# Optimization experiments

Hardware: AMD Instinct MI355X
Metric: run time of the kernel (lower is better)

## Reference

```python
import jax, jax.numpy as jnp
import numpy as np

WH, WW = 7, 7
N = WH * WW
C = 192
H = 6
D = C // H


def _rel_position_index(Wh, Ww):
    # double_step_seq(2*Ww-1, Wh, 1, Ww)
    seq1 = np.arange(0, (2 * Ww - 1) * Wh, 2 * Ww - 1)
    seq2 = np.arange(0, Ww, 1)
    coords = (seq1[:, None] + seq2[None, :]).reshape(1, -1)  # [1, Wh*Ww]
    idx = coords + coords.T                                   # [N, N]
    idx = idx[:, ::-1].copy()                                 # flip(1)
    return idx

REL_IDX = _rel_position_index(WH, WW)  # static int index [N, N]


def setup_inputs() -> dict:
    key = jax.random.key(0)
    ks = jax.random.split(key, 8)
    B = 8192
    nW = 64
    q = jax.random.normal(ks[0], (B, N, C), dtype=jnp.float32)
    kv = jax.random.normal(ks[1], (B, N, C), dtype=jnp.float32)
    mask = jnp.zeros((nW, N, N), dtype=jnp.float32)
    s = 0.02
    Wq = jax.random.normal(ks[2], (C, C), dtype=jnp.float32) * s
    bq = jnp.zeros((C,), dtype=jnp.float32)
    Wkv = jax.random.normal(ks[3], (2 * C, C), dtype=jnp.float32) * s
    bkv = jnp.zeros((2 * C,), dtype=jnp.float32)
    Wo = jax.random.normal(ks[4], (C, C), dtype=jnp.float32) * s
    bo = jnp.zeros((C,), dtype=jnp.float32)
    rpb_table = jax.random.normal(ks[5], ((2 * WH - 1) * (2 * WW - 1), H), dtype=jnp.float32) * s
    return {"q": q, "kv": kv, "mask": mask, "Wq": Wq, "bq": bq,
            "Wkv": Wkv, "bkv": bkv, "Wo": Wo, "bo": bo, "rpb_table": rpb_table}


def reference(q, kv, mask, Wq, bq, Wkv, bkv, Wo, bo, rpb_table):
    B, Nq, _ = q.shape
    Nk = kv.shape[1]
    scale = D ** -0.5
    qh = (q @ Wq.T + bq).reshape(B, Nq, H, D).transpose(0, 2, 1, 3)  # [B,H,Nq,D]
    kvh = (kv @ Wkv.T + bkv).reshape(B, Nk, 2, H, D)
    kh = kvh[:, :, 0].transpose(0, 2, 1, 3)  # [B,H,Nk,D]
    vh = kvh[:, :, 1].transpose(0, 2, 1, 3)
    attn = jnp.einsum('bhqd,bhkd->bhqk', qh * scale, kh)
    bias = rpb_table[REL_IDX.reshape(-1)].reshape(N, N, H).transpose(2, 0, 1)  # [H,N,N]
    attn = attn + bias[None]
    nW = mask.shape[0]
    attn = attn.reshape(B // nW, nW, H, Nq, Nk) + mask[None, :, None]
    attn = attn.reshape(B, H, Nq, Nk)
    attn = jax.nn.softmax(attn, axis=-1)
    x = jnp.einsum('bhqk,bhkd->bhqd', attn, vh).transpose(0, 2, 1, 3).reshape(B, Nq, C)
    return x @ Wo.T + bo
```

## Files before the change

### kernel.cpp

```cpp
#include <hip/hip_runtime.h>

#define NTOK 49
#define CDIM 192
#define NHEAD 6
#define HDIM 32

typedef float f32x4 __attribute__((ext_vector_type(4), may_alias));
typedef short b16x8 __attribute__((ext_vector_type(8), may_alias));
typedef short b16x4 __attribute__((ext_vector_type(4), may_alias));

__device__ __forceinline__ f32x4 MFMA(b16x8 a, b16x8 b, f32x4 c) {
  return __builtin_amdgcn_mfma_f32_16x16x32_bf16(a, b, c, 0, 0, 0);
}

__device__ __forceinline__ short f2bf(float f) {
  unsigned u = __builtin_bit_cast(unsigned, f);
  u += 0x7FFFu + ((u >> 16) & 1u);
  return (short)(u >> 16);
}

__device__ __forceinline__ int swz(int row, int col) {
  return row * CDIM + (col ^ ((row & 7) << 3));
}

__global__ void prep_w(const float* __restrict__ Wq, const float* __restrict__ Wkv,
                       const float* __restrict__ Wo, short* __restrict__ wsW) {
  const float scale = 0.17677669529663687f;
  int i = blockIdx.x * 256 + threadIdx.x;
  if (i >= 147456) return;
  float v;
  if (i < 36864)        v = Wq[i] * scale;
  else if (i < 110592)  v = Wkv[i - 36864];
  else                  v = Wo[i - 110592];
  wsW[i] = f2bf(v);
}

__global__ void prep_bias(const float* __restrict__ rpb, float* __restrict__ bias_t) {
  int idx = blockIdx.x * 256 + threadIdx.x;
  if (idx >= NHEAD * NTOK * NTOK) return;
  int h = idx / (NTOK * NTOK);
  int p = idx % (NTOK * NTOK);
  int i = p / NTOK, j = p % NTOK;
  int ci = (i / 7) * 13 + (i % 7);
  int jj = 48 - j;
  int cj = (jj / 7) * 13 + (jj % 7);
  bias_t[idx] = rpb[(ci + cj) * NHEAD + h];
}

__global__ __attribute__((amdgpu_flat_work_group_size(512, 512),
                          amdgpu_waves_per_eu(4))) void wmsa_kernel(
    const float* __restrict__ qg, const float* __restrict__ kvg,
    const float* __restrict__ maskg, const float* __restrict__ bq,
    const float* __restrict__ bkv, const float* __restrict__ bo,
    const short* __restrict__ wsW, const float* __restrict__ bias_t,
    float* __restrict__ outg, int nW) {
  __shared__ short lds[37632];
  short* SH = lds;
  short* VT = lds + 12288;
  short* KH = lds + 25344;
  float* BF = (float*)lds;

  const int b = blockIdx.x;
  const int tid = threadIdx.x;
  const int w = tid >> 6;
  const int lane = tid & 63;
  const int l15 = lane & 15;
  const int lg = lane >> 4;
  const int R = w >> 1, hw = w & 1, h0 = hw * 3;
  const float scale = 0.17677669529663687f;
  const f32x4 zero4 = {0.f, 0.f, 0.f, 0.f};

  const short* WqB = wsW;
  const short* WkvB = wsW + 36864;
  const short* WoB = wsW + 110592;

  const float* qsrc = qg + (size_t)b * (NTOK * CDIM);
  const float* kvsrc = kvg + (size_t)b * (NTOK * CDIM);

  f32x4 qv[6], kvreg[6];
#pragma unroll
  for (int it = 0; it < 6; ++it) {
    int idx = tid + it * 512;
    int r = idx / 48, c4 = idx % 48;
    qv[it] = (r < NTOK) ? *(const f32x4*)(qsrc + r * CDIM + c4 * 4) : zero4;
  }
#pragma unroll
  for (int it = 0; it < 6; ++it) {
    int idx = tid + it * 512;
    int r = idx / 48, c4 = idx % 48;
    kvreg[it] = (r < NTOK) ? *(const f32x4*)(kvsrc + r * CDIM + c4 * 4) : zero4;
  }
#pragma unroll
  for (int it = 0; it < 6; ++it) {
    int idx = tid + it * 512;
    int r = idx / 48, c4 = idx % 48;
    b16x4 o = {f2bf(qv[it][0]), f2bf(qv[it][1]), f2bf(qv[it][2]), f2bf(qv[it][3])};
    *(b16x4*)(SH + swz(r, c4 * 4)) = o;
  }
  __syncthreads();

  f32x4 qacc[6];
#pragma unroll
  for (int t = 0; t < 6; ++t) qacc[t] = zero4;
  {
    b16x8 aq6[6];
#pragma unroll
    for (int kk = 0; kk < 6; ++kk)
      aq6[kk] = *(const b16x8*)(SH + swz(R * 16 + l15, kk * 32 + lg * 8));
#pragma unroll
    for (int t = 0; t < 6; ++t) {
      const int col = (hw * 6 + t) * 16 + l15;
#pragma unroll
      for (int kk = 0; kk < 6; ++kk) {
        b16x8 bw = *(const b16x8*)(WqB + col * CDIM + kk * 32 + lg * 8);
        qacc[t] = MFMA(aq6[kk], bw, qacc[t]);
      }
    }
  }
  __syncthreads();

#pragma unroll
  for (int t = 0; t < 6; ++t) {
    const int col = (hw * 6 + t) * 16 + l15;
    const float bias = bq[col] * scale;
#pragma unroll
    for (int r = 0; r < 4; ++r)
      SH[swz(R * 16 + lg * 4 + r, hw * 96 + t * 16 + l15)] = f2bf(qacc[t][r] + bias);
  }
  b16x8 aq[3];
#pragma unroll
  for (int hh = 0; hh < 3; ++hh)
    aq[hh] = *(const b16x8*)(SH + swz(R * 16 + l15, hw * 96 + hh * 32 + lg * 8));
  __syncthreads();

#pragma unroll
  for (int it = 0; it < 6; ++it) {
    int idx = tid + it * 512;
    int r = idx / 48, c4 = idx % 48;
    b16x4 o = {f2bf(kvreg[it][0]), f2bf(kvreg[it][1]), f2bf(kvreg[it][2]),
               f2bf(kvreg[it][3])};
    *(b16x4*)(SH + swz(r, c4 * 4)) = o;
  }
  __syncthreads();

#pragma unroll
  for (int jj = 0; jj < 3; ++jj) {
    const int nt = w * 3 + jj;
    const int col = nt * 16 + l15;
    f32x4 acc[4];
#pragma unroll
    for (int m = 0; m < 4; ++m) acc[m] = zero4;
#pragma unroll
    for (int kk = 0; kk < 6; ++kk) {
      b16x8 bw = *(const b16x8*)(WkvB + col * CDIM + kk * 32 + lg * 8);
#pragma unroll
      for (int m = 0; m < 4; ++m) {
        b16x8 a = *(const b16x8*)(SH + swz(m * 16 + l15, kk * 32 + lg * 8));
        acc[m] = MFMA(a, bw, acc[m]);
      }
    }
    const float bias = bkv[col];
    if (col < CDIM) {
#pragma unroll
      for (int m = 0; m < 4; ++m)
#pragma unroll
        for (int r = 0; r < 4; ++r)
          KH[swz(m * 16 + lg * 4 + r, col)] = f2bf(acc[m][r] + bias);
    } else {
      const int c = col - CDIM;
#pragma unroll
      for (int m = 0; m < 4; ++m) {
        b16x4 o = {f2bf(acc[m][0] + bias), f2bf(acc[m][1] + bias),
                   f2bf(acc[m][2] + bias), f2bf(acc[m][3] + bias)};
        *(b16x4*)(VT + c * 68 + m * 16 + lg * 4) = o;
      }
    }
  }
  __syncthreads();

  const float* maskw = maskg + (size_t)(b % nW) * (NTOK * NTOK);
  float maskv[4][4];
#pragma unroll
  for (int nt = 0; nt < 4; ++nt) {
    const int cgl = nt * 16 + l15;
#pragma unroll
    for (int r = 0; r < 4; ++r) {
      const int rw = R * 16 + lg * 4 + r;
      maskv[nt][r] = (rw < NTOK && cgl < NTOK) ? maskw[rw * NTOK + cgl] : 0.f;
    }
  }

  f32x4 xh[3][2];
#pragma unroll
  for (int hh = 0; hh < 3; ++hh) {
    xh[hh][0] = zero4;
    xh[hh][1] = zero4;
  }
#pragma unroll
  for (int hh = 0; hh < 3; ++hh) {
    const int h = h0 + hh;
    f32x4 L[4];
#pragma unroll
    for (int nt = 0; nt < 4; ++nt) {
      b16x8 bk = *(const b16x8*)(KH + swz(nt * 16 + l15, h * 32 + lg * 8));
      L[nt] = MFMA(aq[hh], bk, zero4);
    }
    const float* bt = bias_t + h * (NTOK * NTOK);
#pragma unroll
    for (int nt = 0; nt < 4; ++nt) {
      const int cgl = nt * 16 + l15;
#pragma unroll
      for (int r = 0; r < 4; ++r) {
        const int rw = R * 16 + lg * 4 + r;
        if (rw < NTOK && cgl < NTOK) L[nt][r] += bt[rw * NTOK + cgl] + maskv[nt][r];
        else                          L[nt][r] = -1e9f;
      }
    }
#pragma unroll
    for (int r = 0; r < 4; ++r) {
      float m = fmaxf(fmaxf(L[0][r], L[1][r]), fmaxf(L[2][r], L[3][r]));
      m = fmaxf(m, __shfl_xor(m, 1));
      m = fmaxf(m, __shfl_xor(m, 2));
      m = fmaxf(m, __shfl_xor(m, 4));
      m = fmaxf(m, __shfl_xor(m, 8));
      float p0 = __expf(L[0][r] - m), p1 = __expf(L[1][r] - m);
      float p2 = __expf(L[2][r] - m), p3 = __expf(L[3][r] - m);
      float s = p0 + p1 + p2 + p3;
      s += __shfl_xor(s, 1);
      s += __shfl_xor(s, 2);
      s += __shfl_xor(s, 4);
      s += __shfl_xor(s, 8);
      const float is = 1.0f / s;
      L[0][r] = p0 * is; L[1][r] = p1 * is; L[2][r] = p2 * is; L[3][r] = p3 * is;
    }
#pragma unroll
    for (int nt = 0; nt < 4; ++nt)
#pragma unroll
      for (int r = 0; r < 4; ++r)
        SH[swz(R * 16 + lg * 4 + r, hw * 96 + nt * 16 + l15)] = f2bf(L[nt][r]);
#pragma unroll
    for (int kk = 0; kk < 2; ++kk) {
      b16x8 ap = *(const b16x8*)(SH + swz(R * 16 + l15, hw * 96 + kk * 32 + lg * 8));
#pragma unroll
      for (int nv = 0; nv < 2; ++nv) {
        b16x8 bv = *(const b16x8*)(VT + (h * 32 + nv * 16 + l15) * 68 + kk * 32 + lg * 8);
        xh[hh][nv] = MFMA(ap, bv, xh[hh][nv]);
      }
    }
  }
  __syncthreads();
#pragma unroll
  for (int hh = 0; hh < 3; ++hh)
#pragma unroll
    for (int nv = 0; nv < 2; ++nv)
#pragma unroll
      for (int r = 0; r < 4; ++r)
        KH[swz(R * 16 + lg * 4 + r, (h0 + hh) * 32 + nv * 16 + l15)] =
            f2bf(xh[hh][nv][r]);
  __syncthreads();

#pragma unroll
  for (int t = 0; t < 6; ++t) {
    const int pid = w * 6 + t;
    const int j = pid >> 2, m = pid & 3;
    const int col = j * 16 + l15;
    f32x4 oacc = zero4;
#pragma unroll
    for (int kk = 0; kk < 6; ++kk) {
      b16x8 a = *(const b16x8*)(KH + swz(m * 16 + l15, kk * 32 + lg * 8));
      b16x8 bw = *(const b16x8*)(WoB + col * CDIM + kk * 32 + lg * 8);
      oacc = MFMA(a, bw, oacc);
    }
    const float bias = bo[col];
#pragma unroll
    for (int r = 0; r < 4; ++r) {
      const int row = m * 16 + lg * 4 + r;
      if (row < NTOK) BF[row * 204 + col] = oacc[r] + bias;
    }
  }
  __syncthreads();

  float* dst = outg + (size_t)b * (NTOK * CDIM);
#pragma unroll
  for (int t = 0; t < 5; ++t) {
    int idx = tid + t * 512;
    if (idx < NTOK * 48) {
      int row = idx / 48, c4 = idx % 48;
      f32x4 v = *(const f32x4*)(BF + row * 204 + c4 * 4);
      *(f32x4*)(dst + row * CDIM + c4 * 4) = v;
    }
  }
}

extern "C" void kernel_launch(void* const* d_in, const int* in_sizes, int n_in,
                              void* d_out, int out_size, void* d_ws, size_t ws_size,
                              hipStream_t stream) {
  const float* q = (const float*)d_in[0];
  const float* kv = (const float*)d_in[1];
  const float* mask = (const float*)d_in[2];
  const float* Wq = (const float*)d_in[3];
  const float* bq = (const float*)d_in[4];
  const float* Wkv = (const float*)d_in[5];
  const float* bkv = (const float*)d_in[6];
  const float* Wo = (const float*)d_in[7];
  const float* bo = (const float*)d_in[8];
  const float* rpb = (const float*)d_in[9];
  short* wsW = (short*)d_ws;
  float* bias_t = (float*)((char*)d_ws + 294912);

  const int B = in_sizes[0] / (NTOK * CDIM);
  const int nW = in_sizes[2] / (NTOK * NTOK);

  prep_w<<<576, 256, 0, stream>>>(Wq, Wkv, Wo, wsW);
  prep_bias<<<57, 256, 0, stream>>>(rpb, bias_t);
  wmsa_kernel<<<B, 512, 0, stream>>>(q, kv, mask, bq, bkv, bo, wsW, bias_t,
                                     (float*)d_out, nW);
}
```

Measured before the change: 894.4 us.

## Shrink LDS footprint and restructure per-head-pair pipeline for higher occupancy

Result: slower. 1.216 ms (+36.0%).

```diff
diff --git a/kernel.cpp b/kernel.cpp
--- a/kernel.cpp
+++ b/kernel.cpp
@@ -19,8 +19,17 @@
   return (short)(u >> 16);
 }
 
-__device__ __forceinline__ int swz(int row, int col) {
-  return row * CDIM + (col ^ ((row & 7) << 3));
+__device__ __forceinline__ int swz(int r, int c) {
+  return r * 192 + (c ^ ((r & 7) << 3));
+}
+__device__ __forceinline__ int swz64(int r, int c) {
+  return r * 64 + (c ^ ((r & 7) << 3));
+}
+__device__ __forceinline__ int qs(int r, int c) {
+  return r * 96 + (c ^ ((r & 3) << 3));
+}
+__device__ __forceinline__ int ps(int r, int c) {
+  return r * 32 + (c ^ ((r & 3) << 3));
 }
 
 __global__ void prep_w(const float* __restrict__ Wq, const float* __restrict__ Wkv,
@@ -37,27 +46,31 @@
 
 __global__ void prep_bias(const float* __restrict__ rpb, float* __restrict__ bias_t) {
   int idx = blockIdx.x * 256 + threadIdx.x;
-  if (idx >= NHEAD * NTOK * NTOK) return;
-  int h = idx / (NTOK * NTOK);
-  int p = idx % (NTOK * NTOK);
-  int i = p / NTOK, j = p % NTOK;
-  int ci = (i / 7) * 13 + (i % 7);
-  int jj = 48 - j;
-  int cj = (jj / 7) * 13 + (jj % 7);
-  bias_t[idx] = rpb[(ci + cj) * NHEAD + h];
+  if (idx >= NHEAD * NTOK * 64) return;
+  int k = idx & 63;
+  int q = (idx >> 6) % NTOK;
+  int h = idx / (NTOK * 64);
+  float v = -1e9f;
+  if (k < NTOK) {
+    int ci = (q / 7) * 13 + (q % 7);
+    int jj = 48 - k;
+    int cj = (jj / 7) * 13 + (jj % 7);
+    v = rpb[(ci + cj) * NHEAD + h];
+  }
+  bias_t[idx] = v;
 }
 
 __global__ __attribute__((amdgpu_flat_work_group_size(512, 512),
-                          amdgpu_waves_per_eu(4))) void wmsa_kernel(
+                          amdgpu_waves_per_eu(8))) void wmsa_kernel(
     const float* __restrict__ qg, const float* __restrict__ kvg,
     const float* __restrict__ maskg, const float* __restrict__ bq,
     const float* __restrict__ bkv, const float* __restrict__ bo,
     const short* __restrict__ wsW, const float* __restrict__ bias_t,
     float* __restrict__ outg, int nW) {
-  __shared__ short lds[37632];
-  short* SH = lds;
-  short* VT = lds + 12288;
-  short* KH = lds + 25344;
+  __shared__ short lds[20480];
+  short* X = lds;
+  short* KH2 = lds + 12288;
+  short* VT2 = lds + 16384;
   float* BF = (float*)lds;
 
   const int b = blockIdx.x;
@@ -66,8 +79,7 @@
   const int lane = tid & 63;
   const int l15 = lane & 15;
   const int lg = lane >> 4;
-  const int R = w >> 1, hw = w & 1, h0 = hw * 3;
-  const float scale = 0.17677669529663687f;
+  const int R = w >> 1, hw = w & 1;
   const f32x4 zero4 = {0.f, 0.f, 0.f, 0.f};
 
   const short* WqB = wsW;
@@ -76,219 +88,224 @@
 
   const float* qsrc = qg + (size_t)b * (NTOK * CDIM);
   const float* kvsrc = kvg + (size_t)b * (NTOK * CDIM);
-
-  f32x4 qv[6], kvreg[6];
+  const float* maskw = maskg + (size_t)(b % nW) * (NTOK * NTOK);
+
+  const int qrow = R * 16 + l15;
+  const int qc = qrow > 48 ? 48 : qrow;
+
+  b16x8 aq6[6];
+#pragma unroll
+  for (int kk = 0; kk < 6; ++kk) {
+    f32x4 lo = *(const f32x4*)(qsrc + qc * CDIM + kk * 32 + lg * 8);
+    f32x4 hi = *(const f32x4*)(qsrc + qc * CDIM + kk * 32 + lg * 8 + 4);
+    b16x8 a = {f2bf(lo[0]), f2bf(lo[1]), f2bf(lo[2]), f2bf(lo[3]),
+               f2bf(hi[0]), f2bf(hi[1]), f2bf(hi[2]), f2bf(hi[3])};
+    aq6[kk] = a;
+  }
+  f32x4 qacc[6];
+#pragma unroll
+  for (int t = 0; t < 6; ++t) qacc[t] = zero4;
+#pragma unroll
+  for (int t = 0; t < 6; ++t) {
+    const int h = 2 * (t >> 1) + hw;
+    const int col = h * 32 + (t & 1) * 16 + l15;
+#pragma unroll
+    for (int kk = 0; kk < 6; ++kk) {
+      b16x8 bw = *(const b16x8*)(WqB + col * CDIM + kk * 32 + lg * 8);
+      qacc[t] = MFMA(aq6[kk], bw, qacc[t]);
+    }
+  }
+  short* qscr = X + w * 1536;
+#pragma unroll
+  for (int t = 0; t < 6; ++t) {
+    const int h = 2 * (t >> 1) + hw;
+    const int col = h * 32 + (t & 1) * 16 + l15;
+    const float bias = bq[col] * 0.17677669529663687f;
+#pragma unroll
+    for (int rr = 0; rr < 4; ++rr)
+      qscr[qs(lg * 4 + rr, t * 16 + l15)] = f2bf(qacc[t][rr] + bias);
+  }
+  b16x8 aq[3];
+#pragma unroll
+  for (int pp = 0; pp < 3; ++pp)
+    aq[pp] = *(const b16x8*)(qscr + qs(l15, pp * 32 + lg * 8));
+  __syncthreads();
+
 #pragma unroll
   for (int it = 0; it < 6; ++it) {
     int idx = tid + it * 512;
     int r = idx / 48, c4 = idx % 48;
-    qv[it] = (r < NTOK) ? *(const f32x4*)(qsrc + r * CDIM + c4 * 4) : zero4;
-  }
-#pragma unroll
-  for (int it = 0; it < 6; ++it) {
-    int idx = tid + it * 512;
-    int r = idx / 48, c4 = idx % 48;
-    kvreg[it] = (r < NTOK) ? *(const f32x4*)(kvsrc + r * CDIM + c4 * 4) : zero4;
-  }
-#pragma unroll
-  for (int it = 0; it < 6; ++it) {
-    int idx = tid + it * 512;
-    int r = idx / 48, c4 = idx % 48;
-    b16x4 o = {f2bf(qv[it][0]), f2bf(qv[it][1]), f2bf(qv[it][2]), f2bf(qv[it][3])};
-    *(b16x4*)(SH + swz(r, c4 * 4)) = o;
-  }
-  __syncthreads();
-
-  f32x4 qacc[6];
-#pragma unroll
-  for (int t = 0; t < 6; ++t) qacc[t] = zero4;
-  {
-    b16x8 aq6[6];
-#pragma unroll
-    for (int kk = 0; kk < 6; ++kk)
-      aq6[kk] = *(const b16x8*)(SH + swz(R * 16 + l15, kk * 32 + lg * 8));
-#pragma unroll
-    for (int t = 0; t < 6; ++t) {
-      const int col = (hw * 6 + t) * 16 + l15;
-#pragma unroll
-      for (int kk = 0; kk < 6; ++kk) {
-        b16x8 bw = *(const b16x8*)(WqB + col * CDIM + kk * 32 + lg * 8);
-        qacc[t] = MFMA(aq6[kk], bw, qacc[t]);
-      }
-    }
-  }
-  __syncthreads();
-
-#pragma unroll
-  for (int t = 0; t < 6; ++t) {
-    const int col = (hw * 6 + t) * 16 + l15;
-    const float bias = bq[col] * scale;
-#pragma unroll
-    for (int r = 0; r < 4; ++r)
-      SH[swz(R * 16 + lg * 4 + r, hw * 96 + t * 16 + l15)] = f2bf(qacc[t][r] + bias);
-  }
-  b16x8 aq[3];
-#pragma unroll
-  for (int hh = 0; hh < 3; ++hh)
-    aq[hh] = *(const b16x8*)(SH + swz(R * 16 + l15, hw * 96 + hh * 32 + lg * 8));
-  __syncthreads();
-
-#pragma unroll
-  for (int it = 0; it < 6; ++it) {
-    int idx = tid + it * 512;
-    int r = idx / 48, c4 = idx % 48;
-    b16x4 o = {f2bf(kvreg[it][0]), f2bf(kvreg[it][1]), f2bf(kvreg[it][2]),
-               f2bf(kvreg[it][3])};
-    *(b16x4*)(SH + swz(r, c4 * 4)) = o;
-  }
-  __syncthreads();
-
-#pragma unroll
-  for (int jj = 0; jj < 3; ++jj) {
-    const int nt = w * 3 + jj;
-    const int col = nt * 16 + l15;
+    f32x4 v = (r < NTOK) ? *(const f32x4*)(kvsrc + r * CDIM + c4 * 4) : zero4;
+    b16x4 o = {f2bf(v[0]), f2bf(v[1]), f2bf(v[2]), f2bf(v[3])};
+    *(b16x4*)(X + swz(r, c4 * 4)) = o;
+  }
+  __syncthreads();
+
+  b16x8 xbf[3];
+#pragma unroll
+  for (int p = 0; p < 3; ++p) {
+    const int ct = w & 3;
+    const int isV = w >> 2;
+    const int colg = isV * CDIM + p * 64 + ct * 16 + l15;
     f32x4 acc[4];
 #pragma unroll
     for (int m = 0; m < 4; ++m) acc[m] = zero4;
 #pragma unroll
     for (int kk = 0; kk < 6; ++kk) {
-      b16x8 bw = *(const b16x8*)(WkvB + col * CDIM + kk * 32 + lg * 8);
+      b16x8 bw = *(const b16x8*)(WkvB + colg * CDIM + kk * 32 + lg * 8);
 #pragma unroll
       for (int m = 0; m < 4; ++m) {
-        b16x8 a = *(const b16x8*)(SH + swz(m * 16 + l15, kk * 32 + lg * 8));
+        b16x8 a = *(const b16x8*)(X + swz(m * 16 + l15, kk * 32 + lg * 8));
         acc[m] = MFMA(a, bw, acc[m]);
       }
     }
-    const float bias = bkv[col];
-    if (col < CDIM) {
+    const float bias = bkv[colg];
+    if (!isV) {
 #pragma unroll
       for (int m = 0; m < 4; ++m)
 #pragma unroll
-        for (int r = 0; r < 4; ++r)
-          KH[swz(m * 16 + lg * 4 + r, col)] = f2bf(acc[m][r] + bias);
+        for (int rr = 0; rr < 4; ++rr)
+          KH2[swz64(m * 16 + lg * 4 + rr, ct * 16 + l15)] = f2bf(acc[m][rr] + bias);
     } else {
-      const int c = col - CDIM;
 #pragma unroll
       for (int m = 0; m < 4; ++m) {
         b16x4 o = {f2bf(acc[m][0] + bias), f2bf(acc[m][1] + bias),
                    f2bf(acc[m][2] + bias), f2bf(acc[m][3] + bias)};
-        *(b16x4*)(VT + c * 68 + m * 16 + lg * 4) = o;
-      }
-    }
-  }
-  __syncthreads();
-
-  const float* maskw = maskg + (size_t)(b % nW) * (NTOK * NTOK);
-  float maskv[4][4];
-#pragma unroll
-  for (int nt = 0; nt < 4; ++nt) {
-    const int cgl = nt * 16 + l15;
-#pragma unroll
-    for (int r = 0; r < 4; ++r) {
-      const int rw = R * 16 + lg * 4 + r;
-      maskv[nt][r] = (rw < NTOK && cgl < NTOK) ? maskw[rw * NTOK + cgl] : 0.f;
-    }
-  }
-
-  f32x4 xh[3][2];
-#pragma unroll
-  for (int hh = 0; hh < 3; ++hh) {
-    xh[hh][0] = zero4;
-    xh[hh][1] = zero4;
-  }
-#pragma unroll
-  for (int hh = 0; hh < 3; ++hh) {
-    const int h = h0 + hh;
-    f32x4 L[4];
+        *(b16x4*)(VT2 + swz64(ct * 16 + l15, m * 16 + lg * 4)) = o;
+      }
+    }
+    __syncthreads();
+
+    const int h = 2 * p + hw;
+    f32x4 Ls[4];
 #pragma unroll
     for (int nt = 0; nt < 4; ++nt) {
-      b16x8 bk = *(const b16x8*)(KH + swz(nt * 16 + l15, h * 32 + lg * 8));
-      L[nt] = MFMA(aq[hh], bk, zero4);
-    }
-    const float* bt = bias_t + h * (NTOK * NTOK);
+      b16x8 bk = *(const b16x8*)(KH2 + swz64(nt * 16 + l15, hw * 32 + lg * 8));
+      Ls[nt] = MFMA(bk, aq[p], zero4);
+    }
+    const float* bt = bias_t + (h * NTOK + qc) * 64;
 #pragma unroll
     for (int nt = 0; nt < 4; ++nt) {
-      const int cgl = nt * 16 + l15;
-#pragma unroll
-      for (int r = 0; r < 4; ++r) {
-        const int rw = R * 16 + lg * 4 + r;
-        if (rw < NTOK && cgl < NTOK) L[nt][r] += bt[rw * NTOK + cgl] + maskv[nt][r];
-        else                          L[nt][r] = -1e9f;
-      }
-    }
-#pragma unroll
-    for (int r = 0; r < 4; ++r) {
-      float m = fmaxf(fmaxf(L[0][r], L[1][r]), fmaxf(L[2][r], L[3][r]));
-      m = fmaxf(m, __shfl_xor(m, 1));
-      m = fmaxf(m, __shfl_xor(m, 2));
-      m = fmaxf(m, __shfl_xor(m, 4));
-      m = fmaxf(m, __shfl_xor(m, 8));
-      float p0 = __expf(L[0][r] - m), p1 = __expf(L[1][r] - m);
-      float p2 = __expf(L[2][r] - m), p3 = __expf(L[3][r] - m);
-      float s = p0 + p1 + p2 + p3;
-      s += __shfl_xor(s, 1);
-      s += __shfl_xor(s, 2);
-      s += __shfl_xor(s, 4);
-      s += __shfl_xor(s, 8);
-      const float is = 1.0f / s;
-      L[0][r] = p0 * is; L[1][r] = p1 * is; L[2][r] = p2 * is; L[3][r] = p3 * is;
-    }
+      f32x4 bb = *(const f32x4*)(bt + nt * 16 + lg * 4);
+#pragma unroll
+      for (int rr = 0; rr < 4; ++rr) {
+        int kc = nt * 16 + lg * 4 + rr;
+        kc = kc > 48 ? 48 : kc;
+        Ls[nt][rr] += bb[rr] + maskw[qc * NTOK + kc];
+      }
+    }
+    float mx = Ls[0][0];
 #pragma unroll
     for (int nt = 0; nt < 4; ++nt)
 #pragma unroll
-      for (int r = 0; r < 4; ++r)
-        SH[swz(R * 16 + lg * 4 + r, hw * 96 + nt * 16 + l15)] = f2bf(L[nt][r]);
-#pragma unroll
-    for (int kk = 0; kk < 2; ++kk) {
-      b16x8 ap = *(const b16x8*)(SH + swz(R * 16 + l15, hw * 96 + kk * 32 + lg * 8));
+      for (int rr = 0; rr < 4; ++rr) mx = fmaxf(mx, Ls[nt][rr]);
+    mx = fmaxf(mx, __shfl_xor(mx, 16));
+    mx = fmaxf(mx, __shfl_xor(mx, 32));
+    float sum = 0.f;
+#pragma unroll
+    for (int nt = 0; nt < 4; ++nt)
+#pragma unroll
+      for (int rr = 0; rr < 4; ++rr) {
+        Ls[nt][rr] = __expf(Ls[nt][rr] - mx);
+        sum += Ls[nt][rr];
+      }
+    sum += __shfl_xor(sum, 16);
+    sum += __shfl_xor(sum, 32);
+    const float inv = 1.f / sum;
+    __syncthreads();
+
+    short* Pscr = KH2 + w * 512;
+    b16x8 ap[2];
+#pragma unroll
+    for (int kkh = 0; kkh < 2; ++kkh) {
+#pragma unroll
+      for (int nth = 0; nth < 2; ++nth) {
+        const int nt = 2 * kkh + nth;
+        b16x4 o = {f2bf(Ls[nt][0] * inv), f2bf(Ls[nt][1] * inv),
+                   f2bf(Ls[nt][2] * inv), f2bf(Ls[nt][3] * inv)};
+        *(b16x4*)(Pscr + ps(l15, nth * 16 + lg * 4)) = o;
+      }
+      ap[kkh] = *(const b16x8*)(Pscr + ps(l15, lg * 8));
+    }
+    f32x4 xa[2] = {zero4, zero4};
+#pragma unroll
+    for (int kkh = 0; kkh < 2; ++kkh)
 #pragma unroll
       for (int nv = 0; nv < 2; ++nv) {
-        b16x8 bv = *(const b16x8*)(VT + (h * 32 + nv * 16 + l15) * 68 + kk * 32 + lg * 8);
-        xh[hh][nv] = MFMA(ap, bv, xh[hh][nv]);
-      }
-    }
-  }
-  __syncthreads();
-#pragma unroll
-  for (int hh = 0; hh < 3; ++hh)
+        b16x8 bv = *(const b16x8*)(VT2 + swz64(hw * 32 + nv * 16 + l15, kkh * 32 + lg * 8));
+        xa[nv] = MFMA(ap[kkh], bv, xa[nv]);
+      }
+    b16x8 xb = {f2bf(xa[0][0]), f2bf(xa[0][1]), f2bf(xa[0][2]), f2bf(xa[0][3]),
+                f2bf(xa[1][0]), f2bf(xa[1][1]), f2bf(xa[1][2]), f2bf(xa[1][3])};
+    xbf[p] = xb;
+    __syncthreads();
+  }
+
+#pragma unroll
+  for (int p = 0; p < 3; ++p) {
+    const int h = 2 * p + hw;
 #pragma unroll
     for (int nv = 0; nv < 2; ++nv)
 #pragma unroll
-      for (int r = 0; r < 4; ++r)
-        KH[swz(R * 16 + lg * 4 + r, (h0 + hh) * 32 + nv * 16 + l15)] =
-            f2bf(xh[hh][nv][r]);
-  __syncthreads();
-
+      for (int rr = 0; rr < 4; ++rr)
+        X[swz(R * 16 + lg * 4 + rr, h * 32 + nv * 16 + l15)] = xbf[p][nv * 4 + rr];
+  }
+  __syncthreads();
+
+  f32x4 oacc[6];
+#pragma unroll
+  for (int t = 0; t < 6; ++t) oacc[t] = zero4;
 #pragma unroll
   for (int t = 0; t < 6; ++t) {
-    const int pid = w * 6 + t;
-    const int j = pid >> 2, m = pid & 3;
+    const int j = 2 * t + (w >> 2);
+    const int m = w & 3;
     const int col = j * 16 + l15;
-    f32x4 oacc = zero4;
 #pragma unroll
     for (int kk = 0; kk < 6; ++kk) {
-      b16x8 a = *(const b16x8*)(KH + swz(m * 16 + l15, kk * 32 + lg * 8));
+      b16x8 a = *(const b16x8*)(X + swz(m * 16 + l15, kk * 32 + lg * 8));
       b16x8 bw = *(const b16x8*)(WoB + col * CDIM + kk * 32 + lg * 8);
-      oacc = MFMA(a, bw, oacc);
-    }
-    const float bias = bo[col];
-#pragma unroll
-    for (int r = 0; r < 4; ++r) {
-      const int row = m * 16 + lg * 4 + r;
-      if (row < NTOK) BF[row * 204 + col] = oacc[r] + bias;
+      oacc[t] = MFMA(a, bw, oacc[t]);
     }
   }
   __syncthreads();
 
   float* dst = outg + (size_t)b * (NTOK * CDIM);
-#pragma unroll
-  for (int t = 0; t < 5; ++t) {
-    int idx = tid + t * 512;
-    if (idx < NTOK * 48) {
-      int row = idx / 48, c4 = idx % 48;
-      f32x4 v = *(const f32x4*)(BF + row * 204 + c4 * 4);
-      *(f32x4*)(dst + row * CDIM + c4 * 4) = v;
-    }
+  if ((w & 3) < 2) {
+#pragma unroll
+    for (int t = 0; t < 6; ++t) {
+      const int col = (2 * t + (w >> 2)) * 16 + l15;
+      const float bias = bo[col];
+#pragma unroll
+      for (int rr = 0; rr < 4; ++rr)
+        BF[((w & 3) * 16 + lg * 4 + rr) * 192 + col] = oacc[t][rr] + bias;
+    }
+  }
+  __syncthreads();
+#pragma unroll
+  for (int it = 0; it < 3; ++it) {
+    int idx = tid + it * 512;
+    int row = idx / 48, c4 = idx % 48;
+    *(f32x4*)(dst + row * CDIM + c4 * 4) = *(const f32x4*)(BF + row * 192 + c4 * 4);
+  }
+  __syncthreads();
+  if ((w & 3) >= 2) {
+#pragma unroll
+    for (int t = 0; t < 6; ++t) {
+      const int col = (2 * t + (w >> 2)) * 16 + l15;
+      const float bias = bo[col];
+#pragma unroll
+      for (int rr = 0; rr < 4; ++rr)
+        BF[(((w & 3) - 2) * 16 + lg * 4 + rr) * 192 + col] = oacc[t][rr] + bias;
+    }
+  }
+  __syncthreads();
+#pragma unroll
+  for (int it = 0; it < 2; ++it) {
+    int idx = tid + it * 512;
+    int row2 = idx / 48, c4 = idx % 48;
+    if (row2 < 17)
+      *(f32x4*)(dst + (32 + row2) * CDIM + c4 * 4) =
+          *(const f32x4*)(BF + row2 * 192 + c4 * 4);
   }
 }
 
@@ -312,7 +329,7 @@
   const int nW = in_sizes[2] / (NTOK * NTOK);
 
   prep_w<<<576, 256, 0, stream>>>(Wq, Wkv, Wo, wsW);
-  prep_bias<<<57, 256, 0, stream>>>(rpb, bias_t);
+  prep_bias<<<(NHEAD * NTOK * 64 + 255) / 256, 256, 0, stream>>>(rpb, bias_t);
   wmsa_kernel<<<B, 512, 0, stream>>>(q, kv, mask, bq, bkv, bo, wsW, bias_t,
                                      (float*)d_out, nW);
 }
```
